# Performance work log

Measured on AMD Instinct MI355X. Metric: run time of the kernel, lower is better.

Reference implementation:

```python
import jax, jax.numpy as jnp
import numpy as np

DIM = 768
NUM_HEADS = 16
HEAD_DIM = DIM // NUM_HEADS  # 48
SCALE = 1.0 / np.sqrt(HEAD_DIM).astype(np.float32)


def setup_inputs() -> dict:
    key = jax.random.key(0)
    k1, k2, k3 = jax.random.split(key, 3)
    B, S = 4, 2048
    x = jax.random.normal(k1, (B, S, DIM), dtype=jnp.float32)
    # nn.Linear(dim, 3*dim, bias=False): weight stored transposed -> use [in, out]
    w_qkv = jax.random.normal(k2, (DIM, 3 * DIM), dtype=jnp.float32) * (1.0 / np.sqrt(DIM))
    w_proj = jax.random.normal(k3, (DIM, DIM), dtype=jnp.float32) * (1.0 / np.sqrt(DIM))
    b_proj = jnp.zeros((DIM,), dtype=jnp.float32)
    return {"x": x, "w_qkv": w_qkv, "w_proj": w_proj, "b_proj": b_proj}


def reference(x, w_qkv, w_proj, b_proj):
    B, S, D = x.shape
    qkv = x @ w_qkv                                   # [B,S,3D]
    qkv = qkv.reshape(B, S, 3, NUM_HEADS, HEAD_DIM)
    q, k, v = jnp.moveaxis(qkv, 2, 0)                 # each [B,S,H,hd]
    q = q.transpose(0, 2, 1, 3)                       # [B,H,S,hd]
    k = k.transpose(0, 2, 1, 3)
    v = v.transpose(0, 2, 1, 3)
    attn = jnp.einsum('bhqd,bhkd->bhqk', q, k) * SCALE
    attn = jax.nn.softmax(attn, axis=-1)              # dropout: identity (eval mode)
    out = jnp.einsum('bhqk,bhkd->bhqd', attn, v)      # [B,H,S,hd]
    out = out.transpose(0, 2, 1, 3).reshape(B, S, D)
    return out @ w_proj + b_proj
```

## Files before the change

kernel.cpp:

```cpp
#include <hip/hip_runtime.h>
#include <hip/hip_bf16.h>

#define DIMD   768
#define HEADS  16
#define HD     48
#define SEQ    2048
#define BATCH  4
#define NTOK   (BATCH * SEQ)
#define QKVD   (3 * DIMD)

typedef __attribute__((ext_vector_type(8)))  short s16x8;
typedef __attribute__((ext_vector_type(4)))  float f32x4;
typedef __attribute__((ext_vector_type(16))) float f32x16;
typedef unsigned short ushort_t;

static __device__ __forceinline__ unsigned short f2b(float f) {
  union { __hip_bfloat16 b; unsigned short s; } u;
  u.b = __float2bfloat16(f);
  return u.s;
}
static __device__ __forceinline__ float b2f(unsigned short v) {
  union { float f; unsigned u; } x;
  x.u = ((unsigned)v) << 16;
  return x.f;
}
static __device__ __forceinline__ unsigned pk2(float a, float b) {
  return (unsigned)f2b(a) | ((unsigned)f2b(b) << 16);
}

static __device__ __forceinline__ void gload_lds16(const void* g, void* l) {
  __builtin_amdgcn_global_load_lds(
      (const __attribute__((address_space(1))) unsigned int*)g,
      (__attribute__((address_space(3))) unsigned int*)l, 16, 0, 0);
}

#define CVT_NB   (NTOK * DIMD / 8 / 256)
#define TQ_NBX   (QKVD / 32)
#define TQ_NB    (TQ_NBX * (DIMD / 32))
#define TP_NBX   (DIMD / 32)
#define TP_NB    (TP_NBX * (DIMD / 32))

__global__ __launch_bounds__(256) void cvt_all(
    const float* __restrict__ x, ushort_t* __restrict__ xb,
    const float* __restrict__ wq, ushort_t* __restrict__ wqT,
    const float* __restrict__ wp, ushort_t* __restrict__ wpT) {
  __shared__ float T[32][33];
  const int bid = blockIdx.x;
  const int tid = threadIdx.x;

  if (bid < CVT_NB) {
    const int i = bid * 256 + tid;
    float4 a = ((const float4*)x)[i * 2];
    float4 b = ((const float4*)x)[i * 2 + 1];
    s16x8 v;
    v[0] = (short)f2b(a.x); v[1] = (short)f2b(a.y);
    v[2] = (short)f2b(a.z); v[3] = (short)f2b(a.w);
    v[4] = (short)f2b(b.x); v[5] = (short)f2b(b.y);
    v[6] = (short)f2b(b.z); v[7] = (short)f2b(b.w);
    ((s16x8*)xb)[i] = v;
    return;
  }

  const float* in;
  ushort_t* out;
  int R, C, c0, r0;
  if (bid < CVT_NB + TQ_NB) {
    const int b1 = bid - CVT_NB;
    in = wq; out = wqT; R = DIMD; C = QKVD;
    c0 = (b1 % TQ_NBX) * 32; r0 = (b1 / TQ_NBX) * 32;
  } else {
    const int b2 = bid - CVT_NB - TQ_NB;
    in = wp; out = wpT; R = DIMD; C = DIMD;
    c0 = (b2 % TP_NBX) * 32; r0 = (b2 / TP_NBX) * 32;
  }
  const int lc = tid & 31, lr = tid >> 5;
#pragma unroll
  for (int i = 0; i < 4; ++i)
    T[lr + 8 * i][lc] = in[(size_t)(r0 + lr + 8 * i) * C + c0 + lc];
  __syncthreads();
#pragma unroll
  for (int i = 0; i < 4; ++i)
    out[(size_t)(c0 + lr + 8 * i) * R + r0 + lc] = f2b(T[lc][lr + 8 * i]);
}

template <int OUT_BF16>
__global__ __launch_bounds__(256) void gemm_bf16(
    const ushort_t* __restrict__ A, const ushort_t* __restrict__ Bt,
    const float* __restrict__ bias, void* __restrict__ Cout,
    int M, int N, int K) {
  __shared__ __align__(16) ushort_t As[128 * 64];
  __shared__ __align__(16) ushort_t Bs[128 * 64];

  const int tid = threadIdx.x;
  const int lane = tid & 63;
  const int w = tid >> 6;

  const int nwg = gridDim.x * gridDim.y;
  int bx = blockIdx.x, by = blockIdx.y;
  if ((nwg & 7) == 0) {
    const int orig = by * gridDim.x + bx;
    const int cpx = nwg >> 3;
    const int nid = (orig & 7) * cpx + (orig >> 3);
    bx = nid % gridDim.x;
    by = nid / gridDim.x;
  }
  const int m0 = by * 128, n0 = bx * 128;
  const int wm = (w >> 1) * 64, wn = (w & 1) * 64;

  const int c16s = (tid & 7) ^ ((tid >> 3) & 7);
  const ushort_t* aSrc = A + (size_t)(m0 + (tid >> 3)) * K + c16s * 8;
  const ushort_t* bSrc = Bt + (size_t)(n0 + (tid >> 3)) * K + c16s * 8;

  f32x4 acc[4][4];
#pragma unroll
  for (int i = 0; i < 4; ++i)
#pragma unroll
    for (int j = 0; j < 4; ++j) {
      acc[i][j][0] = 0.f; acc[i][j][1] = 0.f;
      acc[i][j][2] = 0.f; acc[i][j][3] = 0.f;
    }

  for (int k0 = 0; k0 < K; k0 += 64) {
    __syncthreads();
#pragma unroll
    for (int r = 0; r < 4; ++r) {
      gload_lds16(aSrc + (size_t)(r * 32) * K + k0,
                  (char*)As + (r * 256 + w * 64) * 16);
      gload_lds16(bSrc + (size_t)(r * 32) * K + k0,
                  (char*)Bs + (r * 256 + w * 64) * 16);
    }
    __syncthreads();

#pragma unroll
    for (int ks = 0; ks < 2; ++ks) {
      s16x8 af[4], bfr[4];
#pragma unroll
      for (int i = 0; i < 4; ++i) {
        const int ar = wm + i * 16 + (lane & 15);
        const int ac = (ks * 4 + (lane >> 4)) ^ (ar & 7);
        af[i] = *(const s16x8*)&As[ar * 64 + ac * 8];
        const int br = wn + i * 16 + (lane & 15);
        const int bc = (ks * 4 + (lane >> 4)) ^ (br & 7);
        bfr[i] = *(const s16x8*)&Bs[br * 64 + bc * 8];
      }
#pragma unroll
      for (int i = 0; i < 4; ++i)
#pragma unroll
        for (int j = 0; j < 4; ++j)
          acc[i][j] = __builtin_amdgcn_mfma_f32_16x16x32_bf16(
              af[i], bfr[j], acc[i][j], 0, 0, 0);
    }
  }

  if (OUT_BF16) {
    ushort_t* C = (ushort_t*)Cout;
#pragma unroll
    for (int i = 0; i < 4; ++i)
#pragma unroll
      for (int j = 0; j < 4; ++j) {
        const int col = n0 + wn + j * 16 + (lane & 15);
#pragma unroll
        for (int r = 0; r < 4; ++r) {
          const int row = m0 + wm + i * 16 + (lane >> 4) * 4 + r;
          C[(size_t)row * N + col] = f2b(acc[i][j][r]);
        }
      }
  } else {
    float* C = (float*)Cout;
#pragma unroll
    for (int i = 0; i < 4; ++i)
#pragma unroll
      for (int j = 0; j < 4; ++j) {
        const int col = n0 + wn + j * 16 + (lane & 15);
        const float bv = bias ? bias[col] : 0.f;
#pragma unroll
        for (int r = 0; r < 4; ++r) {
          const int row = m0 + wm + i * 16 + (lane >> 4) * 4 + r;
          C[(size_t)row * N + col] = acc[i][j][r] + bv;
        }
      }
  }
}

#define KVB 64
#define QPW 32
#define QPB 256
#define NT  (SEQ / KVB)

__global__ __launch_bounds__(512) void attn_mfma(const ushort_t* __restrict__ QKV,
                                                 ushort_t* __restrict__ Aout) {
  const int bh = blockIdx.x;
  const int qt = blockIdx.y;
  const int b = bh >> 4, h = bh & 15;
  const int tid  = threadIdx.x;
  const int w    = tid >> 6;
  const int lane = tid & 63;
  const int l31  = lane & 31;
  const int hi   = lane >> 5;

  __shared__ __align__(16) ushort_t Kfrag[6 * 64 * 8];
  __shared__ __align__(16) ushort_t Vt2[8 * 65 * 8];

  *(uint4*)&Vt2[tid * 8] = make_uint4(0u, 0u, 0u, 0u);
  if (tid < 8) *(uint4*)&Vt2[4096 + tid * 8] = make_uint4(0u, 0u, 0u, 0u);
  __syncthreads();
  if (tid < 64) Vt2[((tid >> 3) * 65 + 48) * 8 + (tid & 7)] = (ushort_t)0x3F80;

  const ushort_t* qkv_b = QKV + (size_t)b * SEQ * QKVD;

  const float qs = 0.14433756729740643f * 1.44269504088896340f;
  const int qrow = qt * QPB + w * QPW + l31;
  const ushort_t* qsrc = qkv_b + (size_t)qrow * QKVD + h * HD;
  s16x8 qf[3];
#pragma unroll
  for (int ks = 0; ks < 3; ++ks) {
    s16x8 raw = *(const s16x8*)(qsrc + ks * 16 + hi * 8);
    s16x8 v;
#pragma unroll
    for (int j = 0; j < 8; ++j) v[j] = (short)f2b(b2f((unsigned short)raw[j]) * qs);
    qf[ks] = v;
  }

  f32x16 o[2];
#pragma unroll
  for (int mt = 0; mt < 2; ++mt)
#pragma unroll
    for (int r = 0; r < 16; ++r) o[mt][r] = 0.f;

  const int srow = lane;
  const int g0 = w;
  const ushort_t* kv0 = qkv_b + (size_t)srow * QKVD + DIMD + h * HD;

  s16x8 ka, va;
  auto loadKV = [&](int kt) {
    if (g0 < 6) {
      const ushort_t* base = kv0 + (size_t)(kt * KVB) * QKVD;
      ka = *(const s16x8*)(base + g0 * 8);
      va = *(const s16x8*)(base + DIMD + g0 * 8);
    }
  };
  auto writeKV = [&]() {
    if (g0 < 6) {
      const int slot = (srow >> 5) * 3 + (g0 >> 1);
      const int pos = (((srow & 31) + ((g0 & 1) << 5)) ^ slot);
      *(s16x8*)&Kfrag[(slot * 64 + pos) * 8] = ka;
      const int kb = srow >> 3, k7 = srow & 7;
#pragma unroll
      for (int j = 0; j < 8; ++j)
        Vt2[(kb * 65 + 8 * g0 + j) * 8 + k7] = (ushort_t)va[j];
    }
  };

  loadKV(0);

  for (int kt = 0; kt < NT; ++kt) {
    __syncthreads();
    writeKV();
    __syncthreads();
    if (kt + 1 < NT) loadKV(kt + 1);

    f32x16 s0, s1;
#pragma unroll
    for (int r = 0; r < 16; ++r) { s0[r] = 0.f; s1[r] = 0.f; }
    __builtin_amdgcn_s_setprio(1);
#pragma unroll
    for (int ks = 0; ks < 3; ++ks) {
      s16x8 a0 = *(const s16x8*)&Kfrag[(ks * 64 + (lane ^ ks)) * 8];
      s0 = __builtin_amdgcn_mfma_f32_32x32x16_bf16(a0, qf[ks], s0, 0, 0, 0);
      s16x8 a1 = *(const s16x8*)&Kfrag[((3 + ks) * 64 + (lane ^ (3 + ks))) * 8];
      s1 = __builtin_amdgcn_mfma_f32_32x32x16_bf16(a1, qf[ks], s1, 0, 0, 0);
    }
    __builtin_amdgcn_s_setprio(0);

    unsigned pw0[8], pw1[8];
#pragma unroll
    for (int g = 0; g < 8; ++g) {
      pw0[g] = pk2(__builtin_amdgcn_exp2f(s0[2 * g]),
                   __builtin_amdgcn_exp2f(s0[2 * g + 1]));
      pw1[g] = pk2(__builtin_amdgcn_exp2f(s1[2 * g]),
                   __builtin_amdgcn_exp2f(s1[2 * g + 1]));
    }

    __builtin_amdgcn_s_setprio(1);
#pragma unroll
    for (int ks = 0; ks < 4; ++ks) {
      unsigned w0 = (ks < 2) ? pw0[4 * (ks & 1) + 0] : pw1[4 * (ks & 1) + 0];
      unsigned w1 = (ks < 2) ? pw0[4 * (ks & 1) + 1] : pw1[4 * (ks & 1) + 1];
      unsigned w2 = (ks < 2) ? pw0[4 * (ks & 1) + 2] : pw1[4 * (ks & 1) + 2];
      unsigned w3 = (ks < 2) ? pw0[4 * (ks & 1) + 3] : pw1[4 * (ks & 1) + 3];
      asm("v_permlane32_swap_b32 %0, %1" : "+v"(w0), "+v"(w2));
      asm("v_permlane32_swap_b32 %0, %1" : "+v"(w1), "+v"(w3));
      union { unsigned u[4]; s16x8 v; } pf;
      pf.u[0] = w0; pf.u[1] = w1; pf.u[2] = w2; pf.u[3] = w3;
      const int kb = 2 * ks + hi;
#pragma unroll
      for (int mt = 0; mt < 2; ++mt) {
        const int hd = mt * 32 + l31;
        s16x8 vfrag = *(const s16x8*)&Vt2[(kb * 65 + hd) * 8];
        o[mt] = __builtin_amdgcn_mfma_f32_32x32x16_bf16(vfrag, pf.v, o[mt], 0, 0, 0);
      }
    }
    __builtin_amdgcn_s_setprio(0);
  }

  const float lsum = __shfl(o[1][8], l31, 64);
  const float inv = 1.f / lsum;
  const int token = qt * QPB + w * QPW + l31;
  ushort_t* dst = Aout + ((size_t)b * SEQ + token) * DIMD + h * HD;
#pragma unroll
  for (int rq = 0; rq < 4; ++rq) {
    const int hd0 = 8 * rq + 4 * hi;
    uint2 pk;
    pk.x = pk2(o[0][4 * rq + 0] * inv, o[0][4 * rq + 1] * inv);
    pk.y = pk2(o[0][4 * rq + 2] * inv, o[0][4 * rq + 3] * inv);
    *(uint2*)(dst + hd0) = pk;
  }
#pragma unroll
  for (int rq = 0; rq < 2; ++rq) {
    const int hd0 = 32 + 8 * rq + 4 * hi;
    uint2 pk;
    pk.x = pk2(o[1][4 * rq + 0] * inv, o[1][4 * rq + 1] * inv);
    pk.y = pk2(o[1][4 * rq + 2] * inv, o[1][4 * rq + 3] * inv);
    *(uint2*)(dst + hd0) = pk;
  }
}

extern "C" void kernel_launch(void* const* d_in, const int* in_sizes, int n_in,
                              void* d_out, int out_size, void* d_ws, size_t ws_size,
                              hipStream_t stream) {
  const float* x      = (const float*)d_in[0];
  const float* w_qkv  = (const float*)d_in[1];
  const float* w_proj = (const float*)d_in[2];
  const float* b_proj = (const float*)d_in[3];
  float* out = (float*)d_out;

  ushort_t* xb     = (ushort_t*)d_ws;
  ushort_t* wqkvT  = xb + (size_t)NTOK * DIMD;
  ushort_t* wprojT = wqkvT + (size_t)QKVD * DIMD;
  ushort_t* qkv    = wprojT + (size_t)DIMD * DIMD;
  ushort_t* att    = qkv + (size_t)NTOK * QKVD;

  cvt_all<<<CVT_NB + TQ_NB + TP_NB, 256, 0, stream>>>(
      x, xb, w_qkv, wqkvT, w_proj, wprojT);

  gemm_bf16<1><<<dim3(QKVD / 128, NTOK / 128), 256, 0, stream>>>(
      xb, wqkvT, nullptr, qkv, NTOK, QKVD, DIMD);

  attn_mfma<<<dim3(BATCH * HEADS, SEQ / QPB), 512, 0, stream>>>(qkv, att);

  gemm_bf16<0><<<dim3(DIMD / 128, NTOK / 128), 256, 0, stream>>>(
      att, wprojT, b_proj, out, NTOK, DIMD, DIMD);
}
```

Baseline: 140.8 us.

## Double-buffer K via direct global-to-LDS loads and interleave QK/PV per half-tile

```diff
diff --git a/kernel.cpp b/kernel.cpp
--- a/kernel.cpp
+++ b/kernel.cpp
@@ -198,7 +198,7 @@
   const int l31  = lane & 31;
   const int hi   = lane >> 5;
 
-  __shared__ __align__(16) ushort_t Kfrag[6 * 64 * 8];
+  __shared__ __align__(16) ushort_t Kfrag[2][6 * 64 * 8];
   __shared__ __align__(16) ushort_t Vt2[8 * 65 * 8];
 
   *(uint4*)&Vt2[tid * 8] = make_uint4(0u, 0u, 0u, 0u);
@@ -227,80 +227,110 @@
 #pragma unroll
     for (int r = 0; r < 16; ++r) o[mt][r] = 0.f;
 
-  const int srow = lane;
-  const int g0 = w;
-  const ushort_t* kv0 = qkv_b + (size_t)srow * QKVD + DIMD + h * HD;
-
-  s16x8 ka, va;
-  auto loadKV = [&](int kt) {
-    if (g0 < 6) {
-      const ushort_t* base = kv0 + (size_t)(kt * KVB) * QKVD;
-      ka = *(const s16x8*)(base + g0 * 8);
-      va = *(const s16x8*)(base + DIMD + g0 * 8);
-    }
+  const int kkey = (w / 3) * 32 + l31;
+  const int kd0  = (w % 3) * 16 + hi * 8;
+  const ushort_t* kSrc = qkv_b + (size_t)kkey * QKVD + DIMD + h * HD + kd0;
+  const ushort_t* vSrc = qkv_b + (size_t)lane * QKVD + 2 * DIMD + h * HD + w * 8;
+
+  s16x8 va;
+  auto issueK = [&](int kt, int buf) {
+    if (w < 6)
+      gload_lds16(kSrc + (size_t)(kt * KVB) * QKVD,
+                  (char*)&Kfrag[buf][0] + w * 1024);
   };
-  auto writeKV = [&]() {
-    if (g0 < 6) {
-      const int slot = (srow >> 5) * 3 + (g0 >> 1);
-      const int pos = (((srow & 31) + ((g0 & 1) << 5)) ^ slot);
-      *(s16x8*)&Kfrag[(slot * 64 + pos) * 8] = ka;
-      const int kb = srow >> 3, k7 = srow & 7;
+  auto loadV = [&](int kt) {
+    if (w < 6) va = *(const s16x8*)(vSrc + (size_t)(kt * KVB) * QKVD);
+  };
+  auto writeV = [&]() {
+    if (w < 6) {
+      const int kb = lane >> 3, k7 = lane & 7;
 #pragma unroll
       for (int j = 0; j < 8; ++j)
-        Vt2[(kb * 65 + 8 * g0 + j) * 8 + k7] = (ushort_t)va[j];
+        Vt2[(kb * 65 + 8 * w + j) * 8 + k7] = (ushort_t)va[j];
     }
   };
 
-  loadKV(0);
+  issueK(0, 0);
+  loadV(0);
 
   for (int kt = 0; kt < NT; ++kt) {
+    const int cur = kt & 1;
     __syncthreads();
-    writeKV();
+    writeV();
     __syncthreads();
-    if (kt + 1 < NT) loadKV(kt + 1);
-
-    f32x16 s0, s1;
-#pragma unroll
-    for (int r = 0; r < 16; ++r) { s0[r] = 0.f; s1[r] = 0.f; }
+    if (kt + 1 < NT) {
+      issueK(kt + 1, cur ^ 1);
+      loadV(kt + 1);
+    }
+    const ushort_t* kf = &Kfrag[cur][0];
+
+    f32x16 s0;
+#pragma unroll
+    for (int r = 0; r < 16; ++r) s0[r] = 0.f;
     __builtin_amdgcn_s_setprio(1);
 #pragma unroll
     for (int ks = 0; ks < 3; ++ks) {
-      s16x8 a0 = *(const s16x8*)&Kfrag[(ks * 64 + (lane ^ ks)) * 8];
+      s16x8 a0 = *(const s16x8*)&kf[(ks * 64 + lane) * 8];
       s0 = __builtin_amdgcn_mfma_f32_32x32x16_bf16(a0, qf[ks], s0, 0, 0, 0);
-      s16x8 a1 = *(const s16x8*)&Kfrag[((3 + ks) * 64 + (lane ^ (3 + ks))) * 8];
+    }
+    __builtin_amdgcn_s_setprio(0);
+#pragma unroll
+    for (int half = 0; half < 2; ++half) {
+      unsigned p0 = pk2(__builtin_amdgcn_exp2f(s0[half * 8 + 0]),
+                        __builtin_amdgcn_exp2f(s0[half * 8 + 1]));
+      unsigned p1 = pk2(__builtin_amdgcn_exp2f(s0[half * 8 + 2]),
+                        __builtin_amdgcn_exp2f(s0[half * 8 + 3]));
+      unsigned p2 = pk2(__builtin_amdgcn_exp2f(s0[half * 8 + 4]),
+                        __builtin_amdgcn_exp2f(s0[half * 8 + 5]));
+      unsigned p3 = pk2(__builtin_amdgcn_exp2f(s0[half * 8 + 6]),
+                        __builtin_amdgcn_exp2f(s0[half * 8 + 7]));
+      asm("v_permlane32_swap_b32 %0, %1" : "+v"(p0), "+v"(p2));
+      asm("v_permlane32_swap_b32 %0, %1" : "+v"(p1), "+v"(p3));
+      union { unsigned u[4]; s16x8 v; } pf;
+      pf.u[0] = p0; pf.u[1] = p1; pf.u[2] = p2; pf.u[3] = p3;
+      const int kb = 2 * half + hi;
+      __builtin_amdgcn_s_setprio(1);
+#pragma unroll
+      for (int mt = 0; mt < 2; ++mt) {
+        s16x8 vfrag = *(const s16x8*)&Vt2[(kb * 65 + mt * 32 + l31) * 8];
+        o[mt] = __builtin_amdgcn_mfma_f32_32x32x16_bf16(vfrag, pf.v, o[mt], 0, 0, 0);
+      }
+      __builtin_amdgcn_s_setprio(0);
+    }
+
+    f32x16 s1;
+#pragma unroll
+    for (int r = 0; r < 16; ++r) s1[r] = 0.f;
+    __builtin_amdgcn_s_setprio(1);
+#pragma unroll
+    for (int ks = 0; ks < 3; ++ks) {
+      s16x8 a1 = *(const s16x8*)&kf[((3 + ks) * 64 + lane) * 8];
       s1 = __builtin_amdgcn_mfma_f32_32x32x16_bf16(a1, qf[ks], s1, 0, 0, 0);
     }
     __builtin_amdgcn_s_setprio(0);
-
-    unsigned pw0[8], pw1[8];
-#pragma unroll
-    for (int g = 0; g < 8; ++g) {
-      pw0[g] = pk2(__builtin_amdgcn_exp2f(s0[2 * g]),
-                   __builtin_amdgcn_exp2f(s0[2 * g + 1]));
-      pw1[g] = pk2(__builtin_amdgcn_exp2f(s1[2 * g]),
-                   __builtin_amdgcn_exp2f(s1[2 * g + 1]));
-    }
-
-    __builtin_amdgcn_s_setprio(1);
-#pragma unroll
-    for (int ks = 0; ks < 4; ++ks) {
-      unsigned w0 = (ks < 2) ? pw0[4 * (ks & 1) + 0] : pw1[4 * (ks & 1) + 0];
-      unsigned w1 = (ks < 2) ? pw0[4 * (ks & 1) + 1] : pw1[4 * (ks & 1) + 1];
-      unsigned w2 = (ks < 2) ? pw0[4 * (ks & 1) + 2] : pw1[4 * (ks & 1) + 2];
-      unsigned w3 = (ks < 2) ? pw0[4 * (ks & 1) + 3] : pw1[4 * (ks & 1) + 3];
-      asm("v_permlane32_swap_b32 %0, %1" : "+v"(w0), "+v"(w2));
-      asm("v_permlane32_swap_b32 %0, %1" : "+v"(w1), "+v"(w3));
+#pragma unroll
+    for (int half = 0; half < 2; ++half) {
+      unsigned p0 = pk2(__builtin_amdgcn_exp2f(s1[half * 8 + 0]),
+                        __builtin_amdgcn_exp2f(s1[half * 8 + 1]));
+      unsigned p1 = pk2(__builtin_amdgcn_exp2f(s1[half * 8 + 2]),
+                        __builtin_amdgcn_exp2f(s1[half * 8 + 3]));
+      unsigned p2 = pk2(__builtin_amdgcn_exp2f(s1[half * 8 + 4]),
+                        __builtin_amdgcn_exp2f(s1[half * 8 + 5]));
+      unsigned p3 = pk2(__builtin_amdgcn_exp2f(s1[half * 8 + 6]),
+                        __builtin_amdgcn_exp2f(s1[half * 8 + 7]));
+      asm("v_permlane32_swap_b32 %0, %1" : "+v"(p0), "+v"(p2));
+      asm("v_permlane32_swap_b32 %0, %1" : "+v"(p1), "+v"(p3));
       union { unsigned u[4]; s16x8 v; } pf;
-      pf.u[0] = w0; pf.u[1] = w1; pf.u[2] = w2; pf.u[3] = w3;
-      const int kb = 2 * ks + hi;
+      pf.u[0] = p0; pf.u[1] = p1; pf.u[2] = p2; pf.u[3] = p3;
+      const int kb = 2 * (2 + half) + hi;
+      __builtin_amdgcn_s_setprio(1);
 #pragma unroll
       for (int mt = 0; mt < 2; ++mt) {
-        const int hd = mt * 32 + l31;
-        s16x8 vfrag = *(const s16x8*)&Vt2[(kb * 65 + hd) * 8];
+        s16x8 vfrag = *(const s16x8*)&Vt2[(kb * 65 + mt * 32 + l31) * 8];
         o[mt] = __builtin_amdgcn_mfma_f32_32x32x16_bf16(vfrag, pf.v, o[mt], 0, 0, 0);
       }
-    }
-    __builtin_amdgcn_s_setprio(0);
+      __builtin_amdgcn_s_setprio(0);
+    }
   }
 
   const float lsum = __shfl(o[1][8], l31, 64);
```

After: 147.5 us. +4.7%, slower.
